# Kernel tuning notes

Hardware: AMD Instinct MI355X
Metric: run time of the kernel (lower is better)

The kernel has to match this reference:

```python
import jax, jax.numpy as jnp
import numpy as np

N_NODES = 100000


def gcn_conv(x, W, b, src, dst, n_nodes):
    # PyG GCNConv: x' = x @ W; symmetric deg^-1/2 normalization with self-loops; scatter-add; + bias
    h = x @ W  # [N, out]
    ones = jnp.ones(dst.shape[0], dtype=h.dtype)
    deg = jax.ops.segment_sum(ones, dst, num_segments=n_nodes)  # in-degree incl. self-loops
    dinv = jnp.where(deg > 0, jax.lax.rsqrt(deg), 0.0)
    norm = dinv[src] * dinv[dst]                      # [E]
    msgs = h[src] * norm[:, None]                     # gather + scale, [E, out]
    out = jax.ops.segment_sum(msgs, dst, num_segments=n_nodes)  # scatter-add
    return out + b


def setup_inputs() -> dict:
    key = jax.random.key(0)
    ks = jax.random.split(key, 8)
    n, e, din, dh, dout = N_NODES, 1600000, 32, 64, 5
    x = jax.random.normal(ks[0], (n, din), dtype=jnp.float32)
    edge_index = jax.random.randint(ks[1], (2, e), 0, n, dtype=jnp.int64)
    W1 = jax.random.normal(ks[2], (din, dh), dtype=jnp.float32) * (1.0 / np.sqrt(din))
    b1 = jax.random.normal(ks[3], (dh,), dtype=jnp.float32) * 0.02
    W2 = jax.random.normal(ks[4], (dh, dh), dtype=jnp.float32) * (1.0 / np.sqrt(dh))
    b2 = jax.random.normal(ks[5], (dh,), dtype=jnp.float32) * 0.02
    Wfc = jax.random.normal(ks[6], (dh, dout), dtype=jnp.float32) * (1.0 / np.sqrt(dh))
    bfc = jax.random.normal(ks[7], (dout,), dtype=jnp.float32) * 0.02
    return {"x": x, "edge_index": edge_index, "W1": W1, "b1": b1,
            "W2": W2, "b2": b2, "Wfc": Wfc, "bfc": bfc}


def reference(x, edge_index, W1, b1, W2, b2, Wfc, bfc):
    n = x.shape[0]
    loops = jnp.arange(n, dtype=edge_index.dtype)
    src = jnp.concatenate([edge_index[0], loops])  # add self-loops (PyG default)
    dst = jnp.concatenate([edge_index[1], loops])
    h = jax.nn.relu(gcn_conv(x, W1, b1, src, dst, n))
    h = jax.nn.relu(gcn_conv(h, W2, b2, src, dst, n))
    g = jnp.mean(h, axis=0)          # mean pool over nodes, [hidden]
    logits = g @ Wfc + bfc           # [output_dim]
    return jax.nn.log_softmax(logits, axis=0)
```

## Files before the change

### kernel.cpp

```cpp
#include <hip/hip_runtime.h>
#include <math.h>

#define NBLK 256

typedef unsigned int uint;
typedef __attribute__((ext_vector_type(8))) short short8;
typedef __attribute__((ext_vector_type(4))) float f32x4;
typedef __attribute__((ext_vector_type(2))) float f32x2;

#if defined(__has_builtin)
#if __has_builtin(__builtin_amdgcn_cvt_pk_f32_fp8) && __has_builtin(__builtin_amdgcn_cvt_pk_fp8_f32)
#define HW_FP8 1
#endif
#endif
#ifndef HW_FP8
#define HW_FP8 0
#endif

__device__ __forceinline__ uint pack_bf16(float a, float b) {
    uint ua = __float_as_uint(a), ub = __float_as_uint(b);
    ua = (ua + 0x7fffu + ((ua >> 16) & 1u)) >> 16;
    ub = (ub + 0x7fffu + ((ub >> 16) & 1u)) >> 16;
    return ua | (ub << 16);
}

__device__ __forceinline__ uint fp8_enc_sw(float v) {
    uint u = __float_as_uint(v);
    uint s = (u >> 24) & 0x80u;
    uint a = u & 0x7fffffffu;
    if (a < 0x3BF80000u) return s;
    if (a >= 0x43F80000u) return s | 0x7Fu;
    uint r = a + 0x0007FFFFu + ((a >> 20) & 1u);
    uint e8 = (r >> 23) - 120u;
    return s | (e8 << 3) | ((r >> 20) & 7u);
}
__device__ __forceinline__ float fp8_dec_sw(uint b) {
    uint t = b & 0x7fu;
    uint h = ((b & 0x80u) << 8) | (t ? ((t << 7) + 0x2000u) : 0u);
    return (float)__builtin_bit_cast(_Float16, (unsigned short)h);
}

__device__ __forceinline__ uint fp8x2_enc(float a, float b) {
#if HW_FP8
    return (uint)__builtin_amdgcn_cvt_pk_fp8_f32(a, b, 0, false);
#else
    return fp8_enc_sw(a) | (fp8_enc_sw(b) << 8);
#endif
}

#if HW_FP8
#define DEC8ACC(U)                                                         \
    do {                                                                   \
        f32x2 p0 = __builtin_amdgcn_cvt_pk_f32_fp8((int)(U).x, 0);         \
        f32x2 p1 = __builtin_amdgcn_cvt_pk_f32_fp8((int)(U).x, 1);         \
        f32x2 p2 = __builtin_amdgcn_cvt_pk_f32_fp8((int)(U).y, 0);         \
        f32x2 p3 = __builtin_amdgcn_cvt_pk_f32_fp8((int)(U).y, 1);         \
        a0 += p0.x; a1 += p0.y; a2 += p1.x; a3 += p1.y;                    \
        a4 += p2.x; a5 += p2.y; a6 += p3.x; a7 += p3.y;                    \
    } while (0)
#else
#define DEC8ACC(U)                                                         \
    do {                                                                   \
        a0 += fp8_dec_sw((U).x); a1 += fp8_dec_sw((U).x >> 8);             \
        a2 += fp8_dec_sw((U).x >> 16); a3 += fp8_dec_sw((U).x >> 24);      \
        a4 += fp8_dec_sw((U).y); a5 += fp8_dec_sw((U).y >> 8);             \
        a6 += fp8_dec_sw((U).y >> 16); a7 += fp8_dec_sw((U).y >> 24);      \
    } while (0)
#endif


__global__ void pass_hist(const int* __restrict__ dst, int* __restrict__ cnt,
                          int E, int nbucket, int chunk) {
    extern __shared__ int h[];
    int blk = blockIdx.x;
    for (int i = threadIdx.x; i < nbucket; i += blockDim.x) h[i] = 0;
    __syncthreads();
    int lo = blk * chunk, hi = min(lo + chunk, E);
    for (int e = lo + threadIdx.x; e < hi; e += blockDim.x)
        atomicAdd(&h[dst[e] >> 8], 1);
    __syncthreads();
    for (int i = threadIdx.x; i < nbucket; i += blockDim.x)
        cnt[i * NBLK + blk] = h[i];
}

__global__ void row_scan(int* __restrict__ cnt, int* __restrict__ totals) {
    __shared__ int lds[NBLK];
    int b = blockIdx.x, t = threadIdx.x;
    int v = cnt[b * NBLK + t];
    lds[t] = v;
    __syncthreads();
    for (int off = 1; off < NBLK; off <<= 1) {
        int y = (t >= off) ? lds[t - off] : 0;
        __syncthreads();
        lds[t] += y;
        __syncthreads();
    }
    cnt[b * NBLK + t] = lds[t] - v;
    if (t == NBLK - 1) totals[b] = lds[NBLK - 1];
}

__global__ void total_scan(int* __restrict__ totals, int nb) {
    __shared__ int lds[256];
    __shared__ int carry;
    int t = threadIdx.x;
    if (t == 0) carry = 0;
    __syncthreads();
    for (int c = 0; c < nb; c += 256) {
        int v = (c + t < nb) ? totals[c + t] : 0;
        lds[t] = v;
        __syncthreads();
        for (int off = 1; off < 256; off <<= 1) {
            int y = (t >= off) ? lds[t - off] : 0;
            __syncthreads();
            lds[t] += y;
            __syncthreads();
        }
        if (c + t < nb) totals[c + t] = carry + lds[t] - v;
        __syncthreads();
        if (t == 0) carry += lds[255];
        __syncthreads();
    }
    if (t == 0) totals[nb] = carry;
}

__global__ void pass_scatter(const int* __restrict__ src, const int* __restrict__ dst,
                             const int* __restrict__ cnt, const int* __restrict__ totals,
                             int* __restrict__ bucketed, int E, int nbucket, int chunk) {
    extern __shared__ int lcur[];
    int blk = blockIdx.x;
    for (int i = threadIdx.x; i < nbucket; i += blockDim.x)
        lcur[i] = cnt[i * NBLK + blk] + totals[i];
    __syncthreads();
    int lo = blk * chunk, hi = min(lo + chunk, E);
    for (int e = lo + threadIdx.x; e < hi; e += blockDim.x) {
        int s = src[e], d = dst[e];
        int pos = atomicAdd(&lcur[d >> 8], 1);
        bucketed[pos] = (s << 8) | (d & 255);
    }
}

__global__ void bucket_finalize(const int* __restrict__ bucketed, const int* __restrict__ totals,
                                int* __restrict__ rowptr, float* __restrict__ dinv,
                                int* __restrict__ csr_src, const float* __restrict__ x,
                                uint* __restrict__ xfp8, int n) {
    __shared__ int deg[256], sc[256], lcur[256];
    int b = blockIdx.x, t = threadIdx.x;
    int base = totals[b], bend = totals[b + 1];
    deg[t] = 0;
    __syncthreads();
    for (int i = base + t; i < bend; i += 256)
        atomicAdd(&deg[bucketed[i] & 255], 1);
    __syncthreads();
    int v = deg[t];
    sc[t] = v;
    __syncthreads();
    for (int off = 1; off < 256; off <<= 1) {
        int y = (t >= off) ? sc[t - off] : 0;
        __syncthreads();
        sc[t] += y;
        __syncthreads();
    }
    int ex = sc[t] - v;
    lcur[t] = ex;
    int node = b * 256 + t;
    if (node < n) {
        float dfac = rsqrtf((float)(v + 1));
        rowptr[node] = base + ex;
        dinv[node] = dfac;
        const float4* xr = reinterpret_cast<const float4*>(x + (size_t)node * 32);
        uint* xo = xfp8 + (size_t)node * 8;
#pragma unroll
        for (int w = 0; w < 8; ++w) {
            float4 xv = xr[w];
            uint lo = fp8x2_enc(xv.x * dfac, xv.y * dfac);
            uint hi = fp8x2_enc(xv.z * dfac, xv.w * dfac);
            xo[w] = (lo & 0xffffu) | (hi << 16);
        }
    }
    if (b == 0 && t == 0) rowptr[n] = totals[gridDim.x];
    __syncthreads();
    for (int i = base + t; i < bend; i += 256) {
        int p = bucketed[i];
        int pos = atomicAdd(&lcur[p & 255], 1);
        csr_src[base + pos] = p >> 8;
    }
}


__device__ __forceinline__ short8 make_bfrag(const float* __restrict__ W, int kbase, int col) {
    uint w0 = pack_bf16(W[(kbase + 0) * 64 + col], W[(kbase + 1) * 64 + col]);
    uint w1 = pack_bf16(W[(kbase + 2) * 64 + col], W[(kbase + 3) * 64 + col]);
    uint w2 = pack_bf16(W[(kbase + 4) * 64 + col], W[(kbase + 5) * 64 + col]);
    uint w3 = pack_bf16(W[(kbase + 6) * 64 + col], W[(kbase + 7) * 64 + col]);
    uint4 u; u.x = w0; u.y = w1; u.z = w2; u.w = w3;
    return __builtin_bit_cast(short8, u);
}

__global__ __launch_bounds__(256, 4) void agg1_gemm1_fused(
    const int* __restrict__ rowptr, const int* __restrict__ csr_src,
    const float* __restrict__ dinv, const uint* __restrict__ xfp8,
    const float* __restrict__ W, const float* __restrict__ bias,
    uint* __restrict__ outw, int n, int npad) {
    __shared__ uint lds[64 * 16];
    int t = threadIdx.x;
    {
        int v4 = t >> 2, q = t & 3;
        int node = blockIdx.x * 64 + v4;
        const uint* fs = xfp8 + q * 2;
        float a0 = 0.f, a1 = 0.f, a2 = 0.f, a3 = 0.f,
              a4 = 0.f, a5 = 0.f, a6 = 0.f, a7 = 0.f;
        float di = 0.f;
        int k = 0, end = 0;
        if (node < n) {
            k = rowptr[node]; end = rowptr[node + 1];
            di = dinv[node];
            uint2 w = *reinterpret_cast<const uint2*>(fs + (size_t)node * 8);
            DEC8ACC(w);
        }
        for (; k + 4 <= end; k += 4) {
            int s0 = csr_src[k], s1 = csr_src[k + 1], s2 = csr_src[k + 2], s3 = csr_src[k + 3];
            uint2 u0 = *reinterpret_cast<const uint2*>(fs + (size_t)s0 * 8);
            uint2 u1 = *reinterpret_cast<const uint2*>(fs + (size_t)s1 * 8);
            uint2 u2 = *reinterpret_cast<const uint2*>(fs + (size_t)s2 * 8);
            uint2 u3 = *reinterpret_cast<const uint2*>(fs + (size_t)s3 * 8);
            DEC8ACC(u0); DEC8ACC(u1); DEC8ACC(u2); DEC8ACC(u3);
        }
        for (; k < end; ++k) {
            int s = csr_src[k];
            uint2 u = *reinterpret_cast<const uint2*>(fs + (size_t)s * 8);
            DEC8ACC(u);
        }
        uint4 o;
        o.x = pack_bf16(a0 * di, a1 * di);
        o.y = pack_bf16(a2 * di, a3 * di);
        o.z = pack_bf16(a4 * di, a5 * di);
        o.w = pack_bf16(a6 * di, a7 * di);
        *reinterpret_cast<uint4*>(&lds[v4 * 16 + q * 4]) = o;
    }
    __syncthreads();
    int lane = t & 63, wv = t >> 6;
    int rowbase = blockIdx.x * 64 + wv * 16;
    int r16 = lane & 15, g4 = lane >> 4;
    short8 a = __builtin_bit_cast(short8,
        *reinterpret_cast<const uint4*>(&lds[(wv * 16 + r16) * 16 + g4 * 4]));
    int kbase = g4 * 8;
    float dr[4];
#pragma unroll
    for (int r = 0; r < 4; ++r) {
        int row = rowbase + g4 * 4 + r;
        dr[r] = (row < n) ? dinv[row] : 0.f;
    }
#pragma unroll
    for (int nt = 0; nt < 4; ++nt) {
        int col = nt * 16 + r16;
        short8 b = make_bfrag(W, kbase, col);
        f32x4 z = {0.f, 0.f, 0.f, 0.f};
        f32x4 acc = __builtin_amdgcn_mfma_f32_16x16x32_bf16(a, b, z, 0, 0, 0);
        float bcol = bias[col];
#pragma unroll
        for (int r = 0; r < 4; ++r) {
            int row = rowbase + g4 * 4 + r;
            float v = fmaxf(acc[r] + bcol, 0.f) * dr[r];
            float vn = __shfl_xor(v, 1);
            uint e = fp8x2_enc(v, vn) & 0xffffu;
            uint e2 = __shfl_xor(e, 2);
            if ((r16 & 3) == 0)
                outw[((size_t)(col >> 5) * npad + row) * 8 + ((col & 31) >> 2)] =
                    e | (e2 << 16);
        }
    }
}

template <int LOG_NSL>
__global__ __launch_bounds__(256, 4) void agg_gather_fp8(
    const int* __restrict__ rowptr, const int* __restrict__ csr_src,
    const float* __restrict__ dinv, const uint* __restrict__ feat,
    uint* __restrict__ out, int n, int npad) {
    int bid = blockIdx.x;
    int slice = bid & ((1 << LOG_NSL) - 1);
    int chunk = bid >> LOG_NSL;
    int node = chunk * 64 + (threadIdx.x >> 2);
    if (node >= n) return;
    int q = threadIdx.x & 3;
    const uint* fs = feat + (size_t)slice * npad * 8 + q * 2;
    int k = rowptr[node], end = rowptr[node + 1];
    float a0 = 0.f, a1 = 0.f, a2 = 0.f, a3 = 0.f, a4 = 0.f, a5 = 0.f, a6 = 0.f, a7 = 0.f;
    {
        uint2 w = *reinterpret_cast<const uint2*>(fs + (size_t)node * 8);
        DEC8ACC(w);
    }
    for (; k + 4 <= end; k += 4) {
        int s0 = csr_src[k], s1 = csr_src[k + 1], s2 = csr_src[k + 2], s3 = csr_src[k + 3];
        uint2 u0 = *reinterpret_cast<const uint2*>(fs + (size_t)s0 * 8);
        uint2 u1 = *reinterpret_cast<const uint2*>(fs + (size_t)s1 * 8);
        uint2 u2 = *reinterpret_cast<const uint2*>(fs + (size_t)s2 * 8);
        uint2 u3 = *reinterpret_cast<const uint2*>(fs + (size_t)s3 * 8);
        DEC8ACC(u0); DEC8ACC(u1); DEC8ACC(u2); DEC8ACC(u3);
    }
    for (; k < end; ++k) {
        int s = csr_src[k];
        uint2 u = *reinterpret_cast<const uint2*>(fs + (size_t)s * 8);
        DEC8ACC(u);
    }
    float di = dinv[node];
    uint4 o;
    o.x = pack_bf16(a0 * di, a1 * di);
    o.y = pack_bf16(a2 * di, a3 * di);
    o.z = pack_bf16(a4 * di, a5 * di);
    o.w = pack_bf16(a6 * di, a7 * di);
    *reinterpret_cast<uint4*>(
        out + ((size_t)((slice << 1) + (q >> 1)) * npad + node) * 8 + (q & 1) * 4) = o;
}

__global__ __launch_bounds__(256) void gemm2_mfma_pool(const uint* __restrict__ A,
                                                       const float* __restrict__ W,
                                                       const float* __restrict__ bias,
                                                       float* __restrict__ pool_part,
                                                       int n, int npad) {
    __shared__ float sblk[64];
    int t = threadIdx.x;
    if (t < 64) sblk[t] = 0.f;
    __syncthreads();
    int lane = t & 63, wv = t >> 6;
    int rowbase = blockIdx.x * 64 + wv * 16;
    int r16 = lane & 15, g4 = lane >> 4;
    size_t roff = (size_t)(rowbase + r16) * 8 + (g4 & 1) * 4;
    size_t sstride = (size_t)npad * 8;
    short8 a0 = __builtin_bit_cast(short8,
        *reinterpret_cast<const uint4*>(A + (size_t)(g4 >> 1) * sstride + roff));
    short8 a1 = __builtin_bit_cast(short8,
        *reinterpret_cast<const uint4*>(A + (size_t)(2 + (g4 >> 1)) * sstride + roff));
#pragma unroll
    for (int nt = 0; nt < 4; ++nt) {
        int col = nt * 16 + r16;
        short8 b0 = make_bfrag(W, g4 * 8, col);
        short8 b1 = make_bfrag(W, 32 + g4 * 8, col);
        f32x4 z = {0.f, 0.f, 0.f, 0.f};
        f32x4 acc = __builtin_amdgcn_mfma_f32_16x16x32_bf16(a0, b0, z, 0, 0, 0);
        acc = __builtin_amdgcn_mfma_f32_16x16x32_bf16(a1, b1, acc, 0, 0, 0);
        float bcol = bias[col];
        float part = 0.f;
#pragma unroll
        for (int r = 0; r < 4; ++r) {
            int row = rowbase + g4 * 4 + r;
            float v = fmaxf(acc[r] + bcol, 0.f);
            part += (row < n) ? v : 0.f;
        }
        atomicAdd(&sblk[col], part);
    }
    __syncthreads();
    if (t < 64) pool_part[(size_t)blockIdx.x * 64 + t] = sblk[t];
}

__global__ __launch_bounds__(256) void pool_reduce(const float* __restrict__ pool_part,
                                                   int nblk, float* __restrict__ part2) {
    __shared__ float sd[256];
    int t = threadIdx.x;
    int col = t & 63, grp = t >> 6;
    int row0 = blockIdx.x * 4 + grp;
    float acc = 0.f;
    for (int b = row0; b < nblk; b += 256) acc += pool_part[(size_t)b * 64 + col];
    sd[t] = acc;
    __syncthreads();
    if (t < 64)
        part2[(size_t)blockIdx.x * 64 + t] = sd[t] + sd[t + 64] + sd[t + 128] + sd[t + 192];
}

__global__ __launch_bounds__(512) void final_head(const float* __restrict__ part2,
                                                  const float* __restrict__ Wfc,
                                                  const float* __restrict__ bfc,
                                                  float* __restrict__ out, int n) {
    __shared__ float red[512];
    __shared__ float gsh[64];
    __shared__ float logits[5];
    int t = threadIdx.x;
    int col = t & 63, grp = t >> 6;
    float acc = 0.f;
#pragma unroll
    for (int i = 0; i < 8; ++i) acc += part2[(size_t)(grp * 8 + i) * 64 + col];
    red[t] = acc;
    __syncthreads();
    if (t < 64) {
        float s = 0.f;
#pragma unroll
        for (int gI = 0; gI < 8; ++gI) s += red[gI * 64 + t];
        gsh[t] = s;
    }
    __syncthreads();
    if (t < 5) {
        float a = bfc[t];
        float invn = 1.0f / (float)n;
        for (int k = 0; k < 64; ++k) a += (gsh[k] * invn) * Wfc[k * 5 + t];
        logits[t] = a;
    }
    __syncthreads();
    if (t == 0) {
        float m = logits[0];
        for (int i = 1; i < 5; ++i) m = fmaxf(m, logits[i]);
        float s = 0.0f;
        for (int i = 0; i < 5; ++i) s += expf(logits[i] - m);
        float lse = m + logf(s);
        for (int i = 0; i < 5; ++i) out[i] = logits[i] - lse;
    }
}


extern "C" void kernel_launch(void* const* d_in, const int* in_sizes, int n_in,
                              void* d_out, int out_size, void* d_ws, size_t ws_size,
                              hipStream_t stream) {
    const float* x   = (const float*)d_in[0];
    const int*   ei  = (const int*)d_in[1];
    const float* W1  = (const float*)d_in[2];
    const float* b1  = (const float*)d_in[3];
    const float* W2  = (const float*)d_in[4];
    const float* b2  = (const float*)d_in[5];
    const float* Wfc = (const float*)d_in[6];
    const float* bfc = (const float*)d_in[7];
    float* out = (float*)d_out;

    const int n = in_sizes[0] / 32;
    const int E = in_sizes[1] / 2;
    const int* src = ei;
    const int* dst = ei + E;
    const int npad = (n + 63) & ~63;
    const int nbucket = (n + 255) >> 8;
    const int chunk = (E + NBLK - 1) / NBLK;
    const int nchunk = (n + 63) / 64;

    int*   csr_src = (int*)d_ws;
    int*   rowptr  = csr_src + E;
    float* dinv    = (float*)(rowptr + n + 1);
    int*   cnt     = (int*)(dinv + n);
    int*   totals  = cnt + (size_t)nbucket * NBLK;
    size_t offw    = (size_t)(totals + nbucket + 1 - (int*)d_ws);
    offw           = (offw + 3) & ~(size_t)3;
    uint*  xfp8    = (uint*)d_ws + offw;
    uint*  h1fp8   = xfp8 + (size_t)npad * 8;
    uint*  agg2    = h1fp8 + (size_t)2 * npad * 8;
    float* pool_part = (float*)(agg2 + (size_t)4 * npad * 8);
    float* part2   = pool_part + (size_t)nchunk * 64;
    int*   bucketed = (int*)agg2;

    const int B = 256;
    const size_t lds_b = (size_t)nbucket * sizeof(int);

    pass_hist<<<NBLK, B, lds_b, stream>>>(dst, cnt, E, nbucket, chunk);
    row_scan<<<nbucket, NBLK, 0, stream>>>(cnt, totals);
    total_scan<<<1, B, 0, stream>>>(totals, nbucket);
    pass_scatter<<<NBLK, B, lds_b, stream>>>(src, dst, cnt, totals, bucketed, E, nbucket, chunk);
    bucket_finalize<<<nbucket, B, 0, stream>>>(bucketed, totals, rowptr, dinv, csr_src,
                                               x, xfp8, n);

    agg1_gemm1_fused<<<nchunk, B, 0, stream>>>(rowptr, csr_src, dinv, xfp8, W1, b1,
                                               h1fp8, n, npad);

    agg_gather_fp8<1><<<nchunk * 2, B, 0, stream>>>(rowptr, csr_src, dinv, h1fp8, agg2, n, npad);
    gemm2_mfma_pool<<<nchunk, B, 0, stream>>>(agg2, W2, b2, pool_part, n, npad);

    pool_reduce<<<64, B, 0, stream>>>(pool_part, nchunk, part2);
    final_head<<<1, 512, 0, stream>>>(part2, Wfc, bfc, out, n);
}
```

Before: 123.0 us.

## Sort nodes by degree within 64-node groups to balance gather loops

bucket_finalize now ranks each node by in-degree within its 64-node group and writes a permutation into the no-longer-needed cnt buffer. Both aggregation kernels, the fused layer-1 gather+GEMM and the layer-2 gather, process nodes in this permuted order. The aim is that the 16 nodes sharing a wavefront have similar degrees, so fewer lanes sit idle in the neighbour loop. The cost is an extra O(64) ranking loop per thread, an extra perm lookup per node, and less contiguous output stores in the fused kernel.

After: 126.3 us. 2.7% more time.

```diff
diff --git a/kernel.cpp b/kernel.cpp
--- a/kernel.cpp
+++ b/kernel.cpp
@@ -142,7 +142,7 @@
 __global__ void bucket_finalize(const int* __restrict__ bucketed, const int* __restrict__ totals,
                                 int* __restrict__ rowptr, float* __restrict__ dinv,
                                 int* __restrict__ csr_src, const float* __restrict__ x,
-                                uint* __restrict__ xfp8, int n) {
+                                uint* __restrict__ xfp8, int* __restrict__ perm, int n) {
     __shared__ int deg[256], sc[256], lcur[256];
     int b = blockIdx.x, t = threadIdx.x;
     int base = totals[b], bend = totals[b + 1];
@@ -162,6 +162,15 @@
     }
     int ex = sc[t] - v;
     lcur[t] = ex;
+    {
+        int g64 = t & ~63;
+        int rank = 0;
+        for (int j = 0; j < 64; ++j) {
+            int dj = deg[g64 + j];
+            rank += (dj > v || (dj == v && (g64 + j) < t)) ? 1 : 0;
+        }
+        perm[b * 256 + g64 + rank] = b * 256 + t;
+    }
     int node = b * 256 + t;
     if (node < n) {
         float dfac = rsqrtf((float)(v + 1));
@@ -199,22 +208,25 @@
 __global__ __launch_bounds__(256, 4) void agg1_gemm1_fused(
     const int* __restrict__ rowptr, const int* __restrict__ csr_src,
     const float* __restrict__ dinv, const uint* __restrict__ xfp8,
+    const int* __restrict__ perm,
     const float* __restrict__ W, const float* __restrict__ bias,
     uint* __restrict__ outw, int n, int npad) {
     __shared__ uint lds[64 * 16];
+    __shared__ int pidx[64];
     int t = threadIdx.x;
+    if (t < 64) pidx[t] = perm[blockIdx.x * 64 + t];
     {
         int v4 = t >> 2, q = t & 3;
-        int node = blockIdx.x * 64 + v4;
+        int pn = perm[blockIdx.x * 64 + v4];
         const uint* fs = xfp8 + q * 2;
         float a0 = 0.f, a1 = 0.f, a2 = 0.f, a3 = 0.f,
               a4 = 0.f, a5 = 0.f, a6 = 0.f, a7 = 0.f;
         float di = 0.f;
         int k = 0, end = 0;
-        if (node < n) {
-            k = rowptr[node]; end = rowptr[node + 1];
-            di = dinv[node];
-            uint2 w = *reinterpret_cast<const uint2*>(fs + (size_t)node * 8);
+        if (pn < n) {
+            k = rowptr[pn]; end = rowptr[pn + 1];
+            di = dinv[pn];
+            uint2 w = *reinterpret_cast<const uint2*>(fs + (size_t)pn * 8);
             DEC8ACC(w);
         }
         for (; k + 4 <= end; k += 4) {
@@ -239,16 +251,16 @@
     }
     __syncthreads();
     int lane = t & 63, wv = t >> 6;
-    int rowbase = blockIdx.x * 64 + wv * 16;
     int r16 = lane & 15, g4 = lane >> 4;
     short8 a = __builtin_bit_cast(short8,
         *reinterpret_cast<const uint4*>(&lds[(wv * 16 + r16) * 16 + g4 * 4]));
     int kbase = g4 * 8;
+    int pr[4];
     float dr[4];
 #pragma unroll
     for (int r = 0; r < 4; ++r) {
-        int row = rowbase + g4 * 4 + r;
-        dr[r] = (row < n) ? dinv[row] : 0.f;
+        pr[r] = pidx[wv * 16 + g4 * 4 + r];
+        dr[r] = (pr[r] < n) ? dinv[pr[r]] : 0.f;
     }
 #pragma unroll
     for (int nt = 0; nt < 4; ++nt) {
@@ -259,13 +271,12 @@
         float bcol = bias[col];
 #pragma unroll
         for (int r = 0; r < 4; ++r) {
-            int row = rowbase + g4 * 4 + r;
             float v = fmaxf(acc[r] + bcol, 0.f) * dr[r];
             float vn = __shfl_xor(v, 1);
             uint e = fp8x2_enc(v, vn) & 0xffffu;
             uint e2 = __shfl_xor(e, 2);
-            if ((r16 & 3) == 0)
-                outw[((size_t)(col >> 5) * npad + row) * 8 + ((col & 31) >> 2)] =
+            if (pr[r] < n && (r16 & 3) == 0)
+                outw[((size_t)(col >> 5) * npad + pr[r]) * 8 + ((col & 31) >> 2)] =
                     e | (e2 << 16);
         }
     }
@@ -274,12 +285,12 @@
 template <int LOG_NSL>
 __global__ __launch_bounds__(256, 4) void agg_gather_fp8(
     const int* __restrict__ rowptr, const int* __restrict__ csr_src,
-    const float* __restrict__ dinv, const uint* __restrict__ feat,
-    uint* __restrict__ out, int n, int npad) {
+    const float* __restrict__ dinv, const int* __restrict__ perm,
+    const uint* __restrict__ feat, uint* __restrict__ out, int n, int npad) {
     int bid = blockIdx.x;
     int slice = bid & ((1 << LOG_NSL) - 1);
     int chunk = bid >> LOG_NSL;
-    int node = chunk * 64 + (threadIdx.x >> 2);
+    int node = perm[chunk * 64 + (threadIdx.x >> 2)];
     if (node >= n) return;
     int q = threadIdx.x & 3;
     const uint* fs = feat + (size_t)slice * npad * 8 + q * 2;
@@ -440,6 +451,7 @@
     float* pool_part = (float*)(agg2 + (size_t)4 * npad * 8);
     float* part2   = pool_part + (size_t)nchunk * 64;
     int*   bucketed = (int*)agg2;
+    int*   perm    = cnt;
 
     const int B = 256;
     const size_t lds_b = (size_t)nbucket * sizeof(int);
@@ -449,12 +461,13 @@
     total_scan<<<1, B, 0, stream>>>(totals, nbucket);
     pass_scatter<<<NBLK, B, lds_b, stream>>>(src, dst, cnt, totals, bucketed, E, nbucket, chunk);
     bucket_finalize<<<nbucket, B, 0, stream>>>(bucketed, totals, rowptr, dinv, csr_src,
-                                               x, xfp8, n);
-
-    agg1_gemm1_fused<<<nchunk, B, 0, stream>>>(rowptr, csr_src, dinv, xfp8, W1, b1,
+                                               x, xfp8, perm, n);
+
+    agg1_gemm1_fused<<<nchunk, B, 0, stream>>>(rowptr, csr_src, dinv, xfp8, perm, W1, b1,
                                                h1fp8, n, npad);
 
-    agg_gather_fp8<1><<<nchunk * 2, B, 0, stream>>>(rowptr, csr_src, dinv, h1fp8, agg2, n, npad);
+    agg_gather_fp8<1><<<nchunk * 2, B, 0, stream>>>(rowptr, csr_src, dinv, perm, h1fp8,
+                                                    agg2, n, npad);
     gemm2_mfma_pool<<<nchunk, B, 0, stream>>>(agg2, W2, b2, pool_part, n, npad);
 
     pool_reduce<<<64, B, 0, stream>>>(pool_part, nchunk, part2);
```

## Fuse layer-2 gather aggregation with GEMM2 and pooling through swizzled LDS

Applied to the files above, without the earlier changes.

Merges the separate layer-2 fp8 gather kernel and the bf16 GEMM2+pool kernel into one kernel. Each thread now gathers both 32-feature slices for its node, writes the bf16 aggregate into an XOR-swizzled LDS tile, and the MFMA stage reads A fragments from LDS instead of a global intermediate. This drops one launch and the global write and re-read of the agg2 buffer. In exchange, each block does twice the gather work with half the blocks in flight, and the unroll drops from 4 to 2 edges, so latency hiding may suffer.

After: 127.2 us. +3.4%, slower.

```diff
diff --git a/kernel.cpp b/kernel.cpp
--- a/kernel.cpp
+++ b/kernel.cpp
@@ -49,24 +49,25 @@
 }
 
 #if HW_FP8
-#define DEC8ACC(U)                                                         \
+#define DEC8ACCN(U, A0, A1, A2, A3, A4, A5, A6, A7)                        \
     do {                                                                   \
         f32x2 p0 = __builtin_amdgcn_cvt_pk_f32_fp8((int)(U).x, 0);         \
         f32x2 p1 = __builtin_amdgcn_cvt_pk_f32_fp8((int)(U).x, 1);         \
         f32x2 p2 = __builtin_amdgcn_cvt_pk_f32_fp8((int)(U).y, 0);         \
         f32x2 p3 = __builtin_amdgcn_cvt_pk_f32_fp8((int)(U).y, 1);         \
-        a0 += p0.x; a1 += p0.y; a2 += p1.x; a3 += p1.y;                    \
-        a4 += p2.x; a5 += p2.y; a6 += p3.x; a7 += p3.y;                    \
+        A0 += p0.x; A1 += p0.y; A2 += p1.x; A3 += p1.y;                    \
+        A4 += p2.x; A5 += p2.y; A6 += p3.x; A7 += p3.y;                    \
     } while (0)
 #else
-#define DEC8ACC(U)                                                         \
+#define DEC8ACCN(U, A0, A1, A2, A3, A4, A5, A6, A7)                        \
     do {                                                                   \
-        a0 += fp8_dec_sw((U).x); a1 += fp8_dec_sw((U).x >> 8);             \
-        a2 += fp8_dec_sw((U).x >> 16); a3 += fp8_dec_sw((U).x >> 24);      \
-        a4 += fp8_dec_sw((U).y); a5 += fp8_dec_sw((U).y >> 8);             \
-        a6 += fp8_dec_sw((U).y >> 16); a7 += fp8_dec_sw((U).y >> 24);      \
+        A0 += fp8_dec_sw((U).x); A1 += fp8_dec_sw((U).x >> 8);             \
+        A2 += fp8_dec_sw((U).x >> 16); A3 += fp8_dec_sw((U).x >> 24);      \
+        A4 += fp8_dec_sw((U).y); A5 += fp8_dec_sw((U).y >> 8);             \
+        A6 += fp8_dec_sw((U).y >> 16); A7 += fp8_dec_sw((U).y >> 24);      \
     } while (0)
 #endif
+#define DEC8ACC(U) DEC8ACCN(U, a0, a1, a2, a3, a4, a5, a6, a7)
 
 
 __global__ void pass_hist(const int* __restrict__ dst, int* __restrict__ cnt,
@@ -271,73 +272,82 @@
     }
 }
 
-template <int LOG_NSL>
-__global__ __launch_bounds__(256, 4) void agg_gather_fp8(
+__global__ __launch_bounds__(256, 4) void agg2_gemm2_fused(
     const int* __restrict__ rowptr, const int* __restrict__ csr_src,
     const float* __restrict__ dinv, const uint* __restrict__ feat,
-    uint* __restrict__ out, int n, int npad) {
-    int bid = blockIdx.x;
-    int slice = bid & ((1 << LOG_NSL) - 1);
-    int chunk = bid >> LOG_NSL;
-    int node = chunk * 64 + (threadIdx.x >> 2);
-    if (node >= n) return;
-    int q = threadIdx.x & 3;
-    const uint* fs = feat + (size_t)slice * npad * 8 + q * 2;
-    int k = rowptr[node], end = rowptr[node + 1];
-    float a0 = 0.f, a1 = 0.f, a2 = 0.f, a3 = 0.f, a4 = 0.f, a5 = 0.f, a6 = 0.f, a7 = 0.f;
-    {
-        uint2 w = *reinterpret_cast<const uint2*>(fs + (size_t)node * 8);
-        DEC8ACC(w);
-    }
-    for (; k + 4 <= end; k += 4) {
-        int s0 = csr_src[k], s1 = csr_src[k + 1], s2 = csr_src[k + 2], s3 = csr_src[k + 3];
-        uint2 u0 = *reinterpret_cast<const uint2*>(fs + (size_t)s0 * 8);
-        uint2 u1 = *reinterpret_cast<const uint2*>(fs + (size_t)s1 * 8);
-        uint2 u2 = *reinterpret_cast<const uint2*>(fs + (size_t)s2 * 8);
-        uint2 u3 = *reinterpret_cast<const uint2*>(fs + (size_t)s3 * 8);
-        DEC8ACC(u0); DEC8ACC(u1); DEC8ACC(u2); DEC8ACC(u3);
-    }
-    for (; k < end; ++k) {
-        int s = csr_src[k];
-        uint2 u = *reinterpret_cast<const uint2*>(fs + (size_t)s * 8);
-        DEC8ACC(u);
-    }
-    float di = dinv[node];
-    uint4 o;
-    o.x = pack_bf16(a0 * di, a1 * di);
-    o.y = pack_bf16(a2 * di, a3 * di);
-    o.z = pack_bf16(a4 * di, a5 * di);
-    o.w = pack_bf16(a6 * di, a7 * di);
-    *reinterpret_cast<uint4*>(
-        out + ((size_t)((slice << 1) + (q >> 1)) * npad + node) * 8 + (q & 1) * 4) = o;
-}
-
-__global__ __launch_bounds__(256) void gemm2_mfma_pool(const uint* __restrict__ A,
-                                                       const float* __restrict__ W,
-                                                       const float* __restrict__ bias,
-                                                       float* __restrict__ pool_part,
-                                                       int n, int npad) {
+    const float* __restrict__ W, const float* __restrict__ bias,
+    float* __restrict__ pool_part, int n, int npad) {
+    __shared__ uint lds[64 * 32];
     __shared__ float sblk[64];
     int t = threadIdx.x;
     if (t < 64) sblk[t] = 0.f;
+    {
+        int v4 = t >> 2, q = t & 3;
+        int node = blockIdx.x * 64 + v4;
+        const uint* fs0 = feat + q * 2;
+        const uint* fs1 = feat + (size_t)npad * 8 + q * 2;
+        float a0 = 0.f, a1 = 0.f, a2 = 0.f, a3 = 0.f,
+              a4 = 0.f, a5 = 0.f, a6 = 0.f, a7 = 0.f;
+        float c0 = 0.f, c1 = 0.f, c2 = 0.f, c3 = 0.f,
+              c4 = 0.f, c5 = 0.f, c6 = 0.f, c7 = 0.f;
+        float di = 0.f;
+        int k = 0, end = 0;
+        if (node < n) {
+            k = rowptr[node]; end = rowptr[node + 1];
+            di = dinv[node];
+            uint2 w0 = *reinterpret_cast<const uint2*>(fs0 + (size_t)node * 8);
+            uint2 w1 = *reinterpret_cast<const uint2*>(fs1 + (size_t)node * 8);
+            DEC8ACC(w0);
+            DEC8ACCN(w1, c0, c1, c2, c3, c4, c5, c6, c7);
+        }
+        for (; k + 2 <= end; k += 2) {
+            int s0 = csr_src[k], s1 = csr_src[k + 1];
+            uint2 u0a = *reinterpret_cast<const uint2*>(fs0 + (size_t)s0 * 8);
+            uint2 u0b = *reinterpret_cast<const uint2*>(fs1 + (size_t)s0 * 8);
+            uint2 u1a = *reinterpret_cast<const uint2*>(fs0 + (size_t)s1 * 8);
+            uint2 u1b = *reinterpret_cast<const uint2*>(fs1 + (size_t)s1 * 8);
+            DEC8ACC(u0a); DEC8ACC(u1a);
+            DEC8ACCN(u0b, c0, c1, c2, c3, c4, c5, c6, c7);
+            DEC8ACCN(u1b, c0, c1, c2, c3, c4, c5, c6, c7);
+        }
+        for (; k < end; ++k) {
+            int s = csr_src[k];
+            uint2 ua = *reinterpret_cast<const uint2*>(fs0 + (size_t)s * 8);
+            uint2 ub = *reinterpret_cast<const uint2*>(fs1 + (size_t)s * 8);
+            DEC8ACC(ua);
+            DEC8ACCN(ub, c0, c1, c2, c3, c4, c5, c6, c7);
+        }
+        uint4 oa, ob;
+        oa.x = pack_bf16(a0 * di, a1 * di);
+        oa.y = pack_bf16(a2 * di, a3 * di);
+        oa.z = pack_bf16(a4 * di, a5 * di);
+        oa.w = pack_bf16(a6 * di, a7 * di);
+        ob.x = pack_bf16(c0 * di, c1 * di);
+        ob.y = pack_bf16(c2 * di, c3 * di);
+        ob.z = pack_bf16(c4 * di, c5 * di);
+        ob.w = pack_bf16(c6 * di, c7 * di);
+        int ga = q ^ (v4 & 7);
+        int gb = (4 + q) ^ (v4 & 7);
+        *reinterpret_cast<uint4*>(&lds[v4 * 32 + ga * 4]) = oa;
+        *reinterpret_cast<uint4*>(&lds[v4 * 32 + gb * 4]) = ob;
+    }
     __syncthreads();
     int lane = t & 63, wv = t >> 6;
     int rowbase = blockIdx.x * 64 + wv * 16;
     int r16 = lane & 15, g4 = lane >> 4;
-    size_t roff = (size_t)(rowbase + r16) * 8 + (g4 & 1) * 4;
-    size_t sstride = (size_t)npad * 8;
-    short8 a0 = __builtin_bit_cast(short8,
-        *reinterpret_cast<const uint4*>(A + (size_t)(g4 >> 1) * sstride + roff));
-    short8 a1 = __builtin_bit_cast(short8,
-        *reinterpret_cast<const uint4*>(A + (size_t)(2 + (g4 >> 1)) * sstride + roff));
+    int arow = wv * 16 + r16;
+    short8 a0f = __builtin_bit_cast(short8, *reinterpret_cast<const uint4*>(
+        &lds[arow * 32 + (g4 ^ (r16 & 7)) * 4]));
+    short8 a1f = __builtin_bit_cast(short8, *reinterpret_cast<const uint4*>(
+        &lds[arow * 32 + ((4 + g4) ^ (r16 & 7)) * 4]));
 #pragma unroll
     for (int nt = 0; nt < 4; ++nt) {
         int col = nt * 16 + r16;
         short8 b0 = make_bfrag(W, g4 * 8, col);
         short8 b1 = make_bfrag(W, 32 + g4 * 8, col);
         f32x4 z = {0.f, 0.f, 0.f, 0.f};
-        f32x4 acc = __builtin_amdgcn_mfma_f32_16x16x32_bf16(a0, b0, z, 0, 0, 0);
-        acc = __builtin_amdgcn_mfma_f32_16x16x32_bf16(a1, b1, acc, 0, 0, 0);
+        f32x4 acc = __builtin_amdgcn_mfma_f32_16x16x32_bf16(a0f, b0, z, 0, 0, 0);
+        acc = __builtin_amdgcn_mfma_f32_16x16x32_bf16(a1f, b1, acc, 0, 0, 0);
         float bcol = bias[col];
         float part = 0.f;
 #pragma unroll
@@ -436,10 +446,10 @@
     offw           = (offw + 3) & ~(size_t)3;
     uint*  xfp8    = (uint*)d_ws + offw;
     uint*  h1fp8   = xfp8 + (size_t)npad * 8;
-    uint*  agg2    = h1fp8 + (size_t)2 * npad * 8;
-    float* pool_part = (float*)(agg2 + (size_t)4 * npad * 8);
+    uint*  scratch = h1fp8 + (size_t)2 * npad * 8;
+    float* pool_part = (float*)(scratch + E);
     float* part2   = pool_part + (size_t)nchunk * 64;
-    int*   bucketed = (int*)agg2;
+    int*   bucketed = (int*)scratch;
 
     const int B = 256;
     const size_t lds_b = (size_t)nbucket * sizeof(int);
@@ -454,8 +464,8 @@
     agg1_gemm1_fused<<<nchunk, B, 0, stream>>>(rowptr, csr_src, dinv, xfp8, W1, b1,
                                                h1fp8, n, npad);
 
-    agg_gather_fp8<1><<<nchunk * 2, B, 0, stream>>>(rowptr, csr_src, dinv, h1fp8, agg2, n, npad);
-    gemm2_mfma_pool<<<nchunk, B, 0, stream>>>(agg2, W2, b2, pool_part, n, npad);
+    agg2_gemm2_fused<<<nchunk, B, 0, stream>>>(rowptr, csr_src, dinv, h1fp8, W2, b2,
+                                               pool_part, n, npad);
 
     pool_reduce<<<64, B, 0, stream>>>(pool_part, nchunk, part2);
     final_head<<<1, 512, 0, stream>>>(part2, Wfc, bfc, out, n);
```
